# Performance work log

Measured on AMD Instinct MI355X. Metric: run time of the kernel, lower is better.

The kernel has to match this reference:

```python
import jax, jax.numpy as jnp
import numpy as np


def setup_inputs() -> dict:
    key = jax.random.key(0)
    k1, k2 = jax.random.split(key, 2)
    B, C, H, W = 64, 1024, 32, 32
    feature_maps = jax.random.normal(k1, (B, C, H, W), dtype=jnp.float32)
    # 1x1 conv (C -> 1) is just a channel contraction: weight [C], bias [1]
    conv_w = jax.random.normal(k2, (C,), dtype=jnp.float32) * 0.02
    conv_b = jnp.zeros((1,), dtype=jnp.float32)
    M = 768  # int(H * W * drop_rate) = int(1024 * 0.75)
    return {"feature_maps": feature_maps, "conv_w": conv_w, "conv_b": conv_b, "M": M}


def reference(feature_maps, conv_w, conv_b, M):
    # Training-mode ADL forward.
    B, C, H, W = feature_maps.shape
    # 1x1 conv to a single channel + sigmoid -> attention map [B, H, W]
    attn = jax.nn.sigmoid(jnp.einsum('bchw,c->bhw', feature_maps, conv_w) + conv_b[0])
    attn_flat = attn.reshape(B, H * W)
    # drop the top-M most attended spatial locations
    _, topk_idx = jax.lax.top_k(attn_flat, M)            # [B, M]
    drop_mask = jnp.ones_like(attn_flat)
    drop_mask = drop_mask.at[jnp.arange(B)[:, None], topk_idx].set(0.0)
    drop_mask = drop_mask.reshape(B, 1, H, W)
    dropped = feature_maps * drop_mask                   # broadcast over channels
    return dropped, attn.reshape(B, 1, H, W)
```

## Files before the change

### kernel.cpp

```cpp
#include <hip/hip_runtime.h>

typedef float f32x4 __attribute__((ext_vector_type(4)));

#define NB 64
#define NC 1024
#define HW 1024
#define HW4 256

template<int CPC>
__global__ void adl_partial_gemv(const float* __restrict__ fm,
                                 const float* __restrict__ w,
                                 float* __restrict__ partial) {
    const int cchunk = blockIdx.x;
    const int b      = blockIdx.y;
    const int t      = threadIdx.x;
    const f32x4* fm4 = (const f32x4*)fm;
    f32x4 acc = {0.f, 0.f, 0.f, 0.f};
    const int cbase = cchunk * CPC;
    #pragma unroll 8
    for (int ci = 0; ci < CPC; ++ci) {
        const int c = cbase + ci;
        const f32x4 v = fm4[((size_t)(b * NC + c)) * HW4 + t];
        acc += v * w[c];
    }
    ((f32x4*)partial)[((size_t)(cchunk * NB + b)) * HW4 + t] = acc;
}

__global__ void adl_topk_mask(const float* __restrict__ partial,
                              const float* __restrict__ conv_b,
                              const int* __restrict__ Mptr,
                              int ncch,
                              float* __restrict__ attn_out,
                              float* __restrict__ mask) {
    __shared__ f32x4 s_sh4[HW4];
    float* s_sh = (float*)s_sh4;
    const int slice = blockIdx.x;
    const int b     = blockIdx.y;
    const int tid   = threadIdx.x;
    const float bias = conv_b[0];
    #pragma unroll
    for (int q = 0; q < 4; ++q) {
        const int t = q * 256 + tid;
        float s = bias;
        for (int k = 0; k < ncch; ++k)
            s += partial[((size_t)(k * NB + b)) * HW + t];
        s_sh[t] = s;
    }
    __syncthreads();
    const int t = slice * 256 + tid;
    const float sv = s_sh[t];
    const int M = *Mptr;
    int r = 0;
    #pragma unroll 4
    for (int j4 = 0; j4 < HW4; ++j4) {
        const f32x4 v = s_sh4[j4];
        const int j = j4 * 4;
        r += (v.x > sv) || (v.x == sv && (j + 0) < t);
        r += (v.y > sv) || (v.y == sv && (j + 1) < t);
        r += (v.z > sv) || (v.z == sv && (j + 2) < t);
        r += (v.w > sv) || (v.w == sv && (j + 3) < t);
    }
    attn_out[(size_t)b * HW + t] = 1.0f / (1.0f + expf(-sv));
    mask[(size_t)b * HW + t] = (r < M) ? 0.0f : 1.0f;
}

__global__ void adl_apply(const float* __restrict__ fm,
                          const float* __restrict__ mask,
                          float* __restrict__ out) {
    const f32x4* fm4   = (const f32x4*)fm;
    const f32x4* mask4 = (const f32x4*)mask;
    f32x4* out4        = (f32x4*)out;
    const size_t total4 = (size_t)NB * NC * HW4;
    const size_t stride = (size_t)gridDim.x * blockDim.x;
    for (size_t i = (size_t)blockIdx.x * blockDim.x + threadIdx.x;
         i < total4; i += stride) {
        const int hw4 = (int)(i & (HW4 - 1));
        const int b   = (int)(i >> 18);
        const f32x4 m = mask4[b * HW4 + hw4];
        const f32x4 v = fm4[i];
        __builtin_nontemporal_store(v * m, &out4[i]);
    }
}

extern "C" void kernel_launch(void* const* d_in, const int* in_sizes, int n_in,
                              void* d_out, int out_size, void* d_ws, size_t ws_size,
                              hipStream_t stream) {
    const float* fm   = (const float*)d_in[0];
    const float* w    = (const float*)d_in[1];
    const float* bias = (const float*)d_in[2];
    const int*   Mptr = (const int*)d_in[3];

    float* out      = (float*)d_out;
    float* attn_out = out + (size_t)NB * NC * HW;

    const size_t need16 = ((size_t)16 * NB * HW + (size_t)NB * HW) * sizeof(float);
    const int ncch = (ws_size >= need16) ? 16 : 8;
    float* partial = (float*)d_ws;
    float* mask    = partial + (size_t)ncch * NB * HW;

    if (ncch == 16)
        adl_partial_gemv<NC / 16><<<dim3(16, NB), 256, 0, stream>>>(fm, w, partial);
    else
        adl_partial_gemv<NC / 8><<<dim3(8, NB), 256, 0, stream>>>(fm, w, partial);
    adl_topk_mask<<<dim3(4, NB), 256, 0, stream>>>(partial, bias, Mptr, ncch, attn_out, mask);
    adl_apply<<<2048, 256, 0, stream>>>(fm, mask, out);
}
```

Before: 179.0 us.

## Process batch in four chunks so apply pass reuses cached feature maps

Splits the batch into four chunks of 16 and runs gemv, top-k mask and apply per chunk. Each chunk of feature maps is about 64 MB, so it may still sit in the large last-level cache when the apply kernel reads it again. That avoids a second full HBM read of the input. The cost is four times as many kernel launches and smaller grids per launch. The workspace-size check is also replaced with a fixed 32-way channel split.

```diff
diff --git a/kernel.cpp b/kernel.cpp
--- a/kernel.cpp
+++ b/kernel.cpp
@@ -6,44 +6,48 @@
 #define NC 1024
 #define HW 1024
 #define HW4 256
+#define NCHUNK 4
+#define BPC (NB / NCHUNK)
+#define CCH 32
+#define CPC (NC / CCH)
 
-template<int CPC>
-__global__ void adl_partial_gemv(const float* __restrict__ fm,
-                                 const float* __restrict__ w,
-                                 float* __restrict__ partial) {
+__global__ void adl_gemv_chunk(const float* __restrict__ fm_chunk,
+                               const float* __restrict__ w,
+                               float* __restrict__ partial) {
     const int cchunk = blockIdx.x;
-    const int b      = blockIdx.y;
+    const int bb     = blockIdx.y;
     const int t      = threadIdx.x;
-    const f32x4* fm4 = (const f32x4*)fm;
+    const f32x4* fm4 = (const f32x4*)fm_chunk;
     f32x4 acc = {0.f, 0.f, 0.f, 0.f};
     const int cbase = cchunk * CPC;
     #pragma unroll 8
     for (int ci = 0; ci < CPC; ++ci) {
         const int c = cbase + ci;
-        const f32x4 v = fm4[((size_t)(b * NC + c)) * HW4 + t];
+        const f32x4 v = fm4[((size_t)(bb * NC + c)) * HW4 + t];
         acc += v * w[c];
     }
-    ((f32x4*)partial)[((size_t)(cchunk * NB + b)) * HW4 + t] = acc;
+    ((f32x4*)partial)[((size_t)(cchunk * BPC + bb)) * HW4 + t] = acc;
 }
 
-__global__ void adl_topk_mask(const float* __restrict__ partial,
-                              const float* __restrict__ conv_b,
-                              const int* __restrict__ Mptr,
-                              int ncch,
-                              float* __restrict__ attn_out,
-                              float* __restrict__ mask) {
+__global__ void adl_topk_chunk(const float* __restrict__ partial,
+                               const float* __restrict__ conv_b,
+                               const int* __restrict__ Mptr,
+                               int b0,
+                               float* __restrict__ attn_out,
+                               float* __restrict__ mask) {
     __shared__ f32x4 s_sh4[HW4];
     float* s_sh = (float*)s_sh4;
     const int slice = blockIdx.x;
-    const int b     = blockIdx.y;
+    const int bb    = blockIdx.y;
     const int tid   = threadIdx.x;
     const float bias = conv_b[0];
     #pragma unroll
     for (int q = 0; q < 4; ++q) {
         const int t = q * 256 + tid;
         float s = bias;
-        for (int k = 0; k < ncch; ++k)
-            s += partial[((size_t)(k * NB + b)) * HW + t];
+        #pragma unroll 8
+        for (int k = 0; k < CCH; ++k)
+            s += partial[((size_t)(k * BPC + bb)) * HW + t];
         s_sh[t] = s;
     }
     __syncthreads();
@@ -60,23 +64,23 @@
         r += (v.z > sv) || (v.z == sv && (j + 2) < t);
         r += (v.w > sv) || (v.w == sv && (j + 3) < t);
     }
-    attn_out[(size_t)b * HW + t] = 1.0f / (1.0f + expf(-sv));
-    mask[(size_t)b * HW + t] = (r < M) ? 0.0f : 1.0f;
+    attn_out[(size_t)(b0 + bb) * HW + t] = 1.0f / (1.0f + expf(-sv));
+    mask[(size_t)bb * HW + t] = (r < M) ? 0.0f : 1.0f;
 }
 
-__global__ void adl_apply(const float* __restrict__ fm,
-                          const float* __restrict__ mask,
-                          float* __restrict__ out) {
-    const f32x4* fm4   = (const f32x4*)fm;
+__global__ void adl_apply_chunk(const float* __restrict__ fm_chunk,
+                                const float* __restrict__ mask,
+                                float* __restrict__ out_chunk) {
+    const f32x4* fm4   = (const f32x4*)fm_chunk;
     const f32x4* mask4 = (const f32x4*)mask;
-    f32x4* out4        = (f32x4*)out;
-    const size_t total4 = (size_t)NB * NC * HW4;
+    f32x4* out4        = (f32x4*)out_chunk;
+    const size_t total4 = (size_t)BPC * NC * HW4;
     const size_t stride = (size_t)gridDim.x * blockDim.x;
     for (size_t i = (size_t)blockIdx.x * blockDim.x + threadIdx.x;
          i < total4; i += stride) {
         const int hw4 = (int)(i & (HW4 - 1));
-        const int b   = (int)(i >> 18);
-        const f32x4 m = mask4[b * HW4 + hw4];
+        const int bb  = (int)(i >> 18);
+        const f32x4 m = mask4[bb * HW4 + hw4];
         const f32x4 v = fm4[i];
         __builtin_nontemporal_store(v * m, &out4[i]);
     }
@@ -93,15 +97,16 @@
     float* out      = (float*)d_out;
     float* attn_out = out + (size_t)NB * NC * HW;
 
-    const size_t need16 = ((size_t)16 * NB * HW + (size_t)NB * HW) * sizeof(float);
-    const int ncch = (ws_size >= need16) ? 16 : 8;
     float* partial = (float*)d_ws;
-    float* mask    = partial + (size_t)ncch * NB * HW;
+    float* mask    = partial + (size_t)CCH * BPC * HW;
 
-    if (ncch == 16)
-        adl_partial_gemv<NC / 16><<<dim3(16, NB), 256, 0, stream>>>(fm, w, partial);
-    else
-        adl_partial_gemv<NC / 8><<<dim3(8, NB), 256, 0, stream>>>(fm, w, partial);
-    adl_topk_mask<<<dim3(4, NB), 256, 0, stream>>>(partial, bias, Mptr, ncch, attn_out, mask);
-    adl_apply<<<2048, 256, 0, stream>>>(fm, mask, out);
+    const size_t chunk_elems = (size_t)BPC * NC * HW;
+    for (int k = 0; k < NCHUNK; ++k) {
+        const float* fm_chunk  = fm  + (size_t)k * chunk_elems;
+        float*       out_chunk = out + (size_t)k * chunk_elems;
+        adl_gemv_chunk<<<dim3(CCH, BPC), 256, 0, stream>>>(fm_chunk, w, partial);
+        adl_topk_chunk<<<dim3(4, BPC), 256, 0, stream>>>(partial, bias, Mptr,
+                                                         k * BPC, attn_out, mask);
+        adl_apply_chunk<<<2048, 256, 0, stream>>>(fm_chunk, mask, out_chunk);
+    }
 }
```

New measurement: 264.4 us. 47.7% more time.
